# Optimization experiments

Hardware: AMD Instinct MI355X
Metric: run time of the kernel (lower is better)

Reference implementation:

```python
import jax, jax.numpy as jnp
import numpy as np

B, T, IN, H, OUT = 128, 1024, 17, 512, 17


def setup_inputs() -> dict:
    key = jax.random.key(0)
    ks = jax.random.split(key, 11)
    s_in = 1.0 / np.sqrt(H)
    return {
        "x": jax.random.normal(ks[0], (B, T, IN), dtype=jnp.float32),
        "wih0": jax.random.normal(ks[1], (4 * H, IN), dtype=jnp.float32) * s_in,
        "whh0": jax.random.normal(ks[2], (4 * H, H), dtype=jnp.float32) * s_in,
        "bih0": jax.random.normal(ks[3], (4 * H,), dtype=jnp.float32) * s_in,
        "bhh0": jax.random.normal(ks[4], (4 * H,), dtype=jnp.float32) * s_in,
        "wih1": jax.random.normal(ks[5], (4 * H, H), dtype=jnp.float32) * s_in,
        "whh1": jax.random.normal(ks[6], (4 * H, H), dtype=jnp.float32) * s_in,
        "bih1": jax.random.normal(ks[7], (4 * H,), dtype=jnp.float32) * s_in,
        "bhh1": jax.random.normal(ks[8], (4 * H,), dtype=jnp.float32) * s_in,
        "lin_w": jax.random.normal(ks[9], (OUT, H), dtype=jnp.float32) * s_in,
        "lin_b": jax.random.normal(ks[10], (OUT,), dtype=jnp.float32) * s_in,
    }


def _lstm_layer(x, wih, whh, bih, bhh):
    # x: [B, T, D]; gate order i, f, g, o (torch.nn.LSTMCell convention)
    b, _, _ = x.shape
    h = whh.shape[1]
    # Precompute input projection for all timesteps: [B, T, 4H]
    proj = jnp.einsum("btd,gd->btg", x, wih) + bih

    def step(carry, p_t):
        h_t, c_t = carry
        gates = p_t + h_t @ whh.T + bhh  # [B, 4H]
        i, f, g, o = jnp.split(gates, 4, axis=1)
        i = jax.nn.sigmoid(i)
        f = jax.nn.sigmoid(f)
        o = jax.nn.sigmoid(o)
        g = jnp.tanh(g)
        c_t = f * c_t + i * g
        h_t = o * jnp.tanh(c_t)
        return (h_t, c_t), h_t

    h0 = jnp.zeros((b, h), x.dtype)
    c0 = jnp.zeros((b, h), x.dtype)
    _, ys = jax.lax.scan(step, (h0, c0), jnp.swapaxes(proj, 0, 1))  # ys: [T, B, H]
    return jnp.swapaxes(ys, 0, 1)  # [B, T, H]


def reference(x, wih0, whh0, bih0, bhh0, wih1, whh1, bih1, bhh1, lin_w, lin_b):
    y = _lstm_layer(x, wih0, whh0, bih0, bhh0)
    y = _lstm_layer(y, wih1, whh1, bih1, bhh1)
    h_last = y[:, -1, :]  # [B, H]
    return h_last @ lin_w.T + lin_b  # [B, OUT]
```

## Files before the change

kernel.cpp:

```cpp
#include <hip/hip_runtime.h>
#include <cstddef>
#include <cstdint>

typedef unsigned long long ull;
typedef unsigned short u16;
typedef unsigned int u32;
typedef __attribute__((ext_vector_type(8))) short s8v;
typedef __attribute__((ext_vector_type(4))) float f4v;
typedef __attribute__((ext_vector_type(4))) u32 u32x4;

#define GROUPS 8
#define BG     16
#define JS     16
#define TPB    256
#define NT     1024
#define HDIM   512
#define INDIM  17
#define OUTDIM 17
#define BTOT   128

#define AT_LD(p)   __hip_atomic_load((p), __ATOMIC_RELAXED, __HIP_MEMORY_SCOPE_AGENT)
#define AT_ST(p,v) __hip_atomic_store((p), (v), __ATOMIC_RELAXED, __HIP_MEMORY_SCOPE_AGENT)

#define PLANE32 8192
#define WIDX(k, b) ((((k) >> 5) * 512) + ((((k) >> 3) & 3) * 128) + ((b) * 8) + ((k) & 7))

#define RA_OFF     ((size_t)0)
#define RING_BYTES ((size_t)4 * GROUPS * PLANE32 * 4)
#define RB_OFF     (RA_OFF + RING_BYTES)
#define FB32_OFF   (RB_OFF + RING_BYTES)
#define WS_NEEDED  (FB32_OFF + (size_t)BTOT * HDIM * 4)
#define RIX32(sl, gr) (((size_t)(sl) * GROUPS + (gr)) * PLANE32)

#define L_H0   0
#define L_H1   49152
#define L_CTL  65536
#define LDS_SZ 82944

__device__ __forceinline__ u16 f2bf(float f) {
  unsigned int u = __float_as_uint(f);
  u += 0x7FFFu + ((u >> 16) & 1u);
  return (u16)(u >> 16);
}
__device__ __forceinline__ float bf2f(u16 h) {
  return __uint_as_float(((unsigned int)h) << 16);
}
__device__ __forceinline__ float sigm(float x) { return 1.f / (1.f + __expf(-x)); }
__device__ __forceinline__ float tanh_f(float x) { return 2.f / (1.f + __expf(-2.f * x)) - 1.f; }

#define MFMA(a, b, c) __builtin_amdgcn_mfma_f32_16x16x32_bf16((a), (b), (c), 0, 0, 0)

__device__ __forceinline__ ull sc0_read8(const ull* p) {
  ull w;
  asm volatile("global_load_dwordx2 %0, %1, off sc0\n\ts_waitcnt vmcnt(0)"
               : "=&v"(w) : "v"(p) : "memory");
  return w;
}
__device__ __forceinline__ void sc0_read16(const char* base, u32x4 r[16]) {
  asm volatile(
      "global_load_dwordx4 %0, %16, off sc0\n\t"
      "global_load_dwordx4 %1, %16, off offset:1024 sc0\n\t"
      "global_load_dwordx4 %2, %16, off offset:2048 sc0\n\t"
      "global_load_dwordx4 %3, %16, off offset:3072 sc0\n\t"
      "global_load_dwordx4 %4, %17, off sc0\n\t"
      "global_load_dwordx4 %5, %17, off offset:1024 sc0\n\t"
      "global_load_dwordx4 %6, %17, off offset:2048 sc0\n\t"
      "global_load_dwordx4 %7, %17, off offset:3072 sc0\n\t"
      "global_load_dwordx4 %8, %18, off sc0\n\t"
      "global_load_dwordx4 %9, %18, off offset:1024 sc0\n\t"
      "global_load_dwordx4 %10, %18, off offset:2048 sc0\n\t"
      "global_load_dwordx4 %11, %18, off offset:3072 sc0\n\t"
      "global_load_dwordx4 %12, %19, off sc0\n\t"
      "global_load_dwordx4 %13, %19, off offset:1024 sc0\n\t"
      "global_load_dwordx4 %14, %19, off offset:2048 sc0\n\t"
      "global_load_dwordx4 %15, %19, off offset:3072 sc0\n\t"
      "s_waitcnt vmcnt(0)"
      : "=&v"(r[0]), "=&v"(r[1]), "=&v"(r[2]), "=&v"(r[3]),
        "=&v"(r[4]), "=&v"(r[5]), "=&v"(r[6]), "=&v"(r[7]),
        "=&v"(r[8]), "=&v"(r[9]), "=&v"(r[10]), "=&v"(r[11]),
        "=&v"(r[12]), "=&v"(r[13]), "=&v"(r[14]), "=&v"(r[15])
      : "v"(base), "v"(base + 4096), "v"(base + 8192), "v"(base + 12288)
      : "memory");
}

__device__ __forceinline__ void pbar(int* c, int& nbar, int lane) {
  ++nbar;
  if (lane == 0)
    (void)__hip_atomic_fetch_add(c, 1, __ATOMIC_RELEASE, __HIP_MEMORY_SCOPE_WORKGROUP);
  while (__hip_atomic_load(c, __ATOMIC_ACQUIRE, __HIP_MEMORY_SCOPE_WORKGROUP) < 2 * nbar) {}
}

__global__ __launch_bounds__(TPB, 1) void lstm_fused(
    const float* __restrict__ x,
    const float* __restrict__ wih0, const float* __restrict__ whh0,
    const float* __restrict__ bih0, const float* __restrict__ bhh0,
    const float* __restrict__ wih1, const float* __restrict__ whh1,
    const float* __restrict__ bih1, const float* __restrict__ bhh1,
    u32* __restrict__ ringA, u32* __restrict__ ringB,
    float* __restrict__ fb32)
{
  const int bid  = blockIdx.x;
  const int gr   = bid & 7;
  const int wg   = bid >> 3;
  const int j0   = wg * JS;
  const int tid  = threadIdx.x;
  const int wave = tid >> 6;
  const int lane = tid & 63;
  const int n    = lane & 15;
  const int q    = lane >> 4;
  const int k0   = q * 8;
  const int gidx = n & 3;
  const int jl   = n >> 2;

  __shared__ __align__(16) char smem[LDS_SZ];
  int* ctl = (int*)(smem + L_CTL);

  if (tid < 16) ctl[tid] = 0;

  {
    int b_l = tid >> 4, j_l = tid & 15, jgw = j0 + j_l;
    int wo = WIDX(jgw, b_l);
    AT_ST(&ringA[RIX32(0, gr) + wo], 0u);
    AT_ST(&ringB[RIX32(0, gr) + wo], 0u);
  }
  __syncthreads();

  const f4v z = {0.f, 0.f, 0.f, 0.f};
  const int half = wave & 1;
  const int sub = (lane >> 2) * 128 + (lane & 3) * 32;
  const ull TMASK = 0xFFFF0000FFFF0000ULL;

  if (wave < 2) {
    int jown[2];
    float bias[2][4];
    s8v wxh[2], wxl[2];
    s8v whh_[2][16], whl_[2][16];
#pragma unroll
    for (int i = 0; i < 2; ++i) {
      const int jc = wave * 2 + i;
      jown[i] = j0 + jc * 4 + q;
      const float* wr = wih0 + (size_t)(gidx * HDIM + j0 + jc * 4 + jl) * INDIM;
#pragma unroll
      for (int j = 0; j < 8; ++j) {
        int k = k0 + j;
        float v = (k < INDIM) ? wr[k] : 0.f;
        u16 hi = f2bf(v);
        wxh[i][j] = (short)hi;
        wxl[i][j] = (short)f2bf(v - bf2f(hi));
      }
      const float* hr = whh0 + (size_t)(gidx * HDIM + j0 + jc * 4 + jl) * HDIM;
#pragma unroll
      for (int kt = 0; kt < 16; ++kt)
#pragma unroll
        for (int j = 0; j < 8; ++j) {
          float v = hr[kt * 32 + k0 + j];
          u16 hi = f2bf(v);
          whh_[i][kt][j] = (short)hi;
          whl_[i][kt][j] = (short)f2bf(v - bf2f(hi));
        }
#pragma unroll
      for (int g = 0; g < 4; ++g)
        bias[i][g] = bih0[g * HDIM + jown[i]] + bhh0[g * HDIM + jown[i]];
    }
    float cc[2] = {0.f, 0.f};
    int nbar = 0, fast = 1, miss = 0;

    for (int s = 1; s <= NT + 1; ++s) {
      f4v xa[2] = {z, z};
      if (s <= NT) {
        const float* xr = x + ((size_t)(gr * BG + n) * NT + (s - 1)) * INDIM;
        s8v bxh, bxl;
#pragma unroll
        for (int j = 0; j < 8; ++j) {
          int k = k0 + j;
          float v = (k < INDIM) ? xr[k] : 0.f;
          u16 hi = f2bf(v);
          bxh[j] = (short)hi;
          bxl[j] = (short)f2bf(v - bf2f(hi));
        }
#pragma unroll
        for (int i = 0; i < 2; ++i) {
          xa[i] = MFMA(wxh[i], bxh, xa[i]);
          xa[i] = MFMA(wxh[i], bxl, xa[i]);
          xa[i] = MFMA(wxl[i], bxh, xa[i]);
        }
      }
      const int sl3 = (s - 1) % 3;
      {
        const ull* src = (const ull*)(ringA + RIX32((s - 1) & 3, gr)) + half * 2048;
        const ull tg = (ull)(u16)(s - 1);
        const ull pat = (tg << 16) | (tg << 48);
        int it = 0;
        for (;;) {
          ull w;
          if (fast && ((++it) & 7) != 0) w = sc0_read8(src + sub);
          else                           w = AT_LD(src + sub);
          int l1a = __hip_atomic_load(&ctl[7], __ATOMIC_ACQUIRE,
                                      __HIP_MEMORY_SCOPE_WORKGROUP);
          int l1b = __hip_atomic_load(&ctl[8], __ATOMIC_ACQUIRE,
                                      __HIP_MEMORY_SCOPE_WORKGROUP);
          int l1t = l1a < l1b ? l1a : l1b;
          if (__ballot((((w ^ pat) & TMASK) == 0) & (l1t >= s - 4)) == ~0ULL) break;
          if (!fast) __builtin_amdgcn_s_sleep(1);
        }
        u32x4 r[16];
        bool got = false;
        if (fast) {
#pragma unroll 1
          for (int att = 0; att < 2 && !got; ++att) {
            sc0_read16((const char*)src + lane * 16, r);
            ull acc = 0;
#pragma unroll
            for (int i = 0; i < 16; ++i) {
              ull a = ((ull)r[i][1] << 32) | r[i][0];
              ull b = ((ull)r[i][3] << 32) | r[i][2];
              acc |= (a ^ pat) & TMASK;
              acc |= (b ^ pat) & TMASK;
            }
            got = (__ballot(acc == 0) == ~0ULL);
          }
          miss = got ? 0 : miss + 1;
          if (miss >= 4) fast = 0;
        }
        if (!got) {
          for (;;) {
            ull acc = 0;
#pragma unroll
            for (int i = 0; i < 16; ++i) {
              ull a = AT_LD(src + (i * 64 + lane) * 2);
              ull b = AT_LD(src + (i * 64 + lane) * 2 + 1);
              r[i][0] = (u32)a; r[i][1] = (u32)(a >> 32);
              r[i][2] = (u32)b; r[i][3] = (u32)(b >> 32);
              acc |= (a ^ pat) & TMASK;
              acc |= (b ^ pat) & TMASK;
            }
            if (__ballot(acc == 0) == ~0ULL) break;
            __builtin_amdgcn_s_sleep(1);
          }
        }
        char* dst = smem + L_H0 + sl3 * 16384 + half * 8192;
#pragma unroll
        for (int i = 0; i < 16; ++i) {
          ull a = ((ull)r[i][1] << 32) | r[i][0];
          ull b = ((ull)r[i][3] << 32) | r[i][2];
          ull packed = (a & 0xFFFFULL) | ((a >> 16) & 0xFFFF0000ULL)
                     | ((b & 0xFFFFULL) << 32) | (((b >> 16) & 0xFFFF0000ULL) << 32);
          *(ull*)(dst + (i * 64 + lane) * 8) = packed;
        }
      }
      pbar(&ctl[0], nbar, lane);
      if (wave == 0 && lane == 0)
        __hip_atomic_store(&ctl[4 + sl3], s - 1, __ATOMIC_RELEASE,
                           __HIP_MEMORY_SCOPE_WORKGROUP);
      if (s == NT + 1) break;

      const char* sh = smem + L_H0 + sl3 * 16384;
      f4v cHH[2] = {z, z}, cHL[2] = {z, z};
#pragma unroll
      for (int kt = 0; kt < 16; ++kt) {
        s8v bh = *(const s8v*)(sh + kt * 1024 + q * 256 + n * 16);
#pragma unroll
        for (int i = 0; i < 2; ++i) {
          cHH[i] = MFMA(whh_[i][kt], bh, cHH[i]);
          cHL[i] = MFMA(whl_[i][kt], bh, cHL[i]);
        }
      }
      const u32 otag = ((u32)(u16)s) << 16;
      u32* d = ringA + RIX32(s & 3, gr);
#pragma unroll
      for (int ii = 1; ii >= 0; --ii) {
        f4v e = xa[ii] + cHH[ii] + cHL[ii];
        float pi = e[0] + bias[ii][0], pf = e[1] + bias[ii][1];
        float pg = e[2] + bias[ii][2], po = e[3] + bias[ii][3];
        float ig = sigm(pi), fg = sigm(pf), gv = tanh_f(pg), og = sigm(po);
        cc[ii] = fg * cc[ii] + ig * gv;
        AT_ST(d + WIDX(jown[ii], n), otag | (u32)f2bf(og * tanh_f(cc[ii])));
      }
    }
  } else {
    int jown[2];
    float bias[2][4];
    s8v w1x_[2][16], w1h_[2][16];
#pragma unroll
    for (int i = 0; i < 2; ++i) {
      const int jc = (wave - 2) * 2 + i;
      jown[i] = j0 + jc * 4 + q;
      const float* p1 = wih1 + (size_t)(gidx * HDIM + j0 + jc * 4 + jl) * HDIM;
      const float* p2 = whh1 + (size_t)(gidx * HDIM + j0 + jc * 4 + jl) * HDIM;
#pragma unroll
      for (int kt = 0; kt < 16; ++kt)
#pragma unroll
        for (int j = 0; j < 8; ++j) {
          w1x_[i][kt][j] = (short)f2bf(p1[kt * 32 + k0 + j]);
          w1h_[i][kt][j] = (short)f2bf(p2[kt * 32 + k0 + j]);
        }
#pragma unroll
      for (int g = 0; g < 4; ++g)
        bias[i][g] = bih1[g * HDIM + jown[i]] + bhh1[g * HDIM + jown[i]];
    }
    float c1[2] = {0.f, 0.f};
    int nbar = 0, fast = 1, miss = 0;

    for (int t = 1; t <= NT; ++t) {
      {
        const ull* src = (const ull*)(ringB + RIX32((t - 1) & 3, gr)) + half * 2048;
        const ull tg = (ull)(u16)(t - 1);
        const ull pat = (tg << 16) | (tg << 48);
        int it = 0;
        for (;;) {
          ull w;
          if (fast && ((++it) & 7) != 0) w = sc0_read8(src + sub);
          else                           w = AT_LD(src + sub);
          if (__ballot(((w ^ pat) & TMASK) == 0) == ~0ULL) break;
          if (!fast) __builtin_amdgcn_s_sleep(1);
        }
        u32x4 r[16];
        bool got = false;
        if (fast) {
#pragma unroll 1
          for (int att = 0; att < 2 && !got; ++att) {
            sc0_read16((const char*)src + lane * 16, r);
            ull acc = 0;
#pragma unroll
            for (int i = 0; i < 16; ++i) {
              ull a = ((ull)r[i][1] << 32) | r[i][0];
              ull b = ((ull)r[i][3] << 32) | r[i][2];
              acc |= (a ^ pat) & TMASK;
              acc |= (b ^ pat) & TMASK;
            }
            got = (__ballot(acc == 0) == ~0ULL);
          }
          miss = got ? 0 : miss + 1;
          if (miss >= 4) fast = 0;
        }
        if (!got) {
          for (;;) {
            ull acc = 0;
#pragma unroll
            for (int i = 0; i < 16; ++i) {
              ull a = AT_LD(src + (i * 64 + lane) * 2);
              ull b = AT_LD(src + (i * 64 + lane) * 2 + 1);
              r[i][0] = (u32)a; r[i][1] = (u32)(a >> 32);
              r[i][2] = (u32)b; r[i][3] = (u32)(b >> 32);
              acc |= (a ^ pat) & TMASK;
              acc |= (b ^ pat) & TMASK;
            }
            if (__ballot(acc == 0) == ~0ULL) break;
            __builtin_amdgcn_s_sleep(1);
          }
        }
        char* dst = smem + L_H1 + half * 8192;
#pragma unroll
        for (int i = 0; i < 16; ++i) {
          ull a = ((ull)r[i][1] << 32) | r[i][0];
          ull b = ((ull)r[i][3] << 32) | r[i][2];
          ull packed = (a & 0xFFFFULL) | ((a >> 16) & 0xFFFF0000ULL)
                     | ((b & 0xFFFFULL) << 32) | (((b >> 16) & 0xFFFF0000ULL) << 32);
          *(ull*)(dst + (i * 64 + lane) * 8) = packed;
        }
      }
      pbar(&ctl[1], nbar, lane);
      const char* th = smem + L_H1;
      f4v dHH[2] = {z, z};
#pragma unroll
      for (int kt = 0; kt < 16; ++kt) {
        s8v bh = *(const s8v*)(th + kt * 1024 + q * 256 + n * 16);
#pragma unroll
        for (int i = 0; i < 2; ++i) dHH[i] = MFMA(w1h_[i][kt], bh, dHH[i]);
      }
      const int sl3 = t % 3;
      while (__hip_atomic_load(&ctl[4 + sl3], __ATOMIC_ACQUIRE,
                               __HIP_MEMORY_SCOPE_WORKGROUP) < t) {}
      const char* sh = smem + L_H0 + sl3 * 16384;
      f4v eHH[2] = {z, z};
#pragma unroll
      for (int kt = 0; kt < 16; ++kt) {
        s8v bh = *(const s8v*)(sh + kt * 1024 + q * 256 + n * 16);
#pragma unroll
        for (int i = 0; i < 2; ++i) eHH[i] = MFMA(w1x_[i][kt], bh, eHH[i]);
      }
      if (lane == 0)
        __hip_atomic_store(&ctl[7 + (wave & 1)], t, __ATOMIC_RELEASE,
                           __HIP_MEMORY_SCOPE_WORKGROUP);
      const u32 otag = ((u32)(u16)t) << 16;
      u32* d = ringB + RIX32(t & 3, gr);
#pragma unroll
      for (int ii = 1; ii >= 0; --ii) {
        f4v e = dHH[ii] + eHH[ii];
        float pi = e[0] + bias[ii][0], pf = e[1] + bias[ii][1];
        float pg = e[2] + bias[ii][2], po = e[3] + bias[ii][3];
        float ig = sigm(pi), fg = sigm(pf), gv = tanh_f(pg), og = sigm(po);
        c1[ii] = fg * c1[ii] + ig * gv;
        float h = og * tanh_f(c1[ii]);
        AT_ST(d + WIDX(jown[ii], n), otag | (u32)f2bf(h));
        if (t == NT)
          AT_ST((u32*)&fb32[(size_t)(gr * BG + n) * HDIM + jown[ii]],
                __float_as_uint(h));
      }
    }
  }
}

__global__ void final_linear(const float* __restrict__ fb32,
                             const float* __restrict__ lin_w,
                             const float* __restrict__ lin_b,
                             float* __restrict__ out) {
  int b = blockIdx.x, o = threadIdx.x;
  if (o < OUTDIM) {
    float acc = lin_b[o];
    const u32* hr = (const u32*)(fb32 + (size_t)b * HDIM);
    for (int j = 0; j < HDIM; ++j) {
      float h = __uint_as_float(AT_LD(hr + j));
      acc += h * lin_w[(size_t)o * HDIM + j];
    }
    out[b * OUTDIM + o] = acc;
  }
}

__global__ void sentinel_kernel(float* __restrict__ out, int nv) {
  int i = blockIdx.x * TPB + threadIdx.x;
  if (i < nv) out[i] = 1e30f;
}

extern "C" void kernel_launch(void* const* d_in, const int* in_sizes, int n_in,
                              void* d_out, int out_size, void* d_ws, size_t ws_size,
                              hipStream_t stream) {
  (void)in_sizes; (void)n_in;
  const float* x     = (const float*)d_in[0];
  const float* wih0  = (const float*)d_in[1];
  const float* whh0  = (const float*)d_in[2];
  const float* bih0  = (const float*)d_in[3];
  const float* bhh0  = (const float*)d_in[4];
  const float* wih1  = (const float*)d_in[5];
  const float* whh1  = (const float*)d_in[6];
  const float* bih1  = (const float*)d_in[7];
  const float* bhh1  = (const float*)d_in[8];
  const float* lin_w = (const float*)d_in[9];
  const float* lin_b = (const float*)d_in[10];
  float* out = (float*)d_out;
  char* ws = (char*)d_ws;

  if (ws_size < WS_NEEDED) {
    sentinel_kernel<<<(out_size + TPB - 1) / TPB, TPB, 0, stream>>>(out, out_size);
    return;
  }

  u32* ringA  = (u32*)(ws + RA_OFF);
  u32* ringB  = (u32*)(ws + RB_OFF);
  float* fb32 = (float*)(ws + FB32_OFF);

  lstm_fused<<<256, TPB, 0, stream>>>(x, wih0, whh0, bih0, bhh0,
                                      wih1, whh1, bih1, bhh1,
                                      ringA, ringB, fb32);
  final_linear<<<BTOT, 64, 0, stream>>>(fb32, lin_w, lin_b, out);
}
```

Measured before the change: 5.696 ms.

## Stage hidden-state publishes through LDS and drop sc0 fast-path polling

Each wave now writes its gate outputs into a small per-wave LDS staging area and then publishes them to the global ring with one coalesced 64-bit atomic store per lane. Before, each lane issued scattered 32-bit atomic stores. The inline-asm sc0 read fast path and its miss-tracking fallback are removed, so polling always uses plain relaxed atomic loads with s_sleep backoff. This is meant to cut the count and scatter of cross-block global writes on the per-step critical path. The cost is an extra LDS round trip plus a waitcnt in every step, and possibly slower consumer polling without the sc0 loads.

```diff
diff --git a/kernel.cpp b/kernel.cpp
--- a/kernel.cpp
+++ b/kernel.cpp
@@ -7,7 +7,6 @@
 typedef unsigned int u32;
 typedef __attribute__((ext_vector_type(8))) short s8v;
 typedef __attribute__((ext_vector_type(4))) float f4v;
-typedef __attribute__((ext_vector_type(4))) u32 u32x4;
 
 #define GROUPS 8
 #define BG     16
@@ -34,7 +33,8 @@
 
 #define L_H0   0
 #define L_H1   49152
-#define L_CTL  65536
+#define L_STG  65536
+#define L_CTL  67584
 #define LDS_SZ 82944
 
 __device__ __forceinline__ u16 f2bf(float f) {
@@ -49,39 +49,6 @@
 __device__ __forceinline__ float tanh_f(float x) { return 2.f / (1.f + __expf(-2.f * x)) - 1.f; }
 
 #define MFMA(a, b, c) __builtin_amdgcn_mfma_f32_16x16x32_bf16((a), (b), (c), 0, 0, 0)
-
-__device__ __forceinline__ ull sc0_read8(const ull* p) {
-  ull w;
-  asm volatile("global_load_dwordx2 %0, %1, off sc0\n\ts_waitcnt vmcnt(0)"
-               : "=&v"(w) : "v"(p) : "memory");
-  return w;
-}
-__device__ __forceinline__ void sc0_read16(const char* base, u32x4 r[16]) {
-  asm volatile(
-      "global_load_dwordx4 %0, %16, off sc0\n\t"
-      "global_load_dwordx4 %1, %16, off offset:1024 sc0\n\t"
-      "global_load_dwordx4 %2, %16, off offset:2048 sc0\n\t"
-      "global_load_dwordx4 %3, %16, off offset:3072 sc0\n\t"
-      "global_load_dwordx4 %4, %17, off sc0\n\t"
-      "global_load_dwordx4 %5, %17, off offset:1024 sc0\n\t"
-      "global_load_dwordx4 %6, %17, off offset:2048 sc0\n\t"
-      "global_load_dwordx4 %7, %17, off offset:3072 sc0\n\t"
-      "global_load_dwordx4 %8, %18, off sc0\n\t"
-      "global_load_dwordx4 %9, %18, off offset:1024 sc0\n\t"
-      "global_load_dwordx4 %10, %18, off offset:2048 sc0\n\t"
-      "global_load_dwordx4 %11, %18, off offset:3072 sc0\n\t"
-      "global_load_dwordx4 %12, %19, off sc0\n\t"
-      "global_load_dwordx4 %13, %19, off offset:1024 sc0\n\t"
-      "global_load_dwordx4 %14, %19, off offset:2048 sc0\n\t"
-      "global_load_dwordx4 %15, %19, off offset:3072 sc0\n\t"
-      "s_waitcnt vmcnt(0)"
-      : "=&v"(r[0]), "=&v"(r[1]), "=&v"(r[2]), "=&v"(r[3]),
-        "=&v"(r[4]), "=&v"(r[5]), "=&v"(r[6]), "=&v"(r[7]),
-        "=&v"(r[8]), "=&v"(r[9]), "=&v"(r[10]), "=&v"(r[11]),
-        "=&v"(r[12]), "=&v"(r[13]), "=&v"(r[14]), "=&v"(r[15])
-      : "v"(base), "v"(base + 4096), "v"(base + 8192), "v"(base + 12288)
-      : "memory");
-}
 
 __device__ __forceinline__ void pbar(int* c, int& nbar, int lane) {
   ++nbar;
@@ -114,6 +81,7 @@
 
   __shared__ __align__(16) char smem[LDS_SZ];
   int* ctl = (int*)(smem + L_CTL);
+  u32* stg = (u32*)(smem + L_STG + (wave & 1) * 512 + (wave >> 1) * 1024);
 
   if (tid < 16) ctl[tid] = 0;
 
@@ -127,6 +95,7 @@
 
   const f4v z = {0.f, 0.f, 0.f, 0.f};
   const int half = wave & 1;
+  const int pub = (wg >> 1) * 256 + ((wg & 1) * 2 + (wave & 1)) * 64;
   const int sub = (lane >> 2) * 128 + (lane & 3) * 32;
   const ull TMASK = 0xFFFF0000FFFF0000ULL;
 
@@ -163,7 +132,7 @@
         bias[i][g] = bih0[g * HDIM + jown[i]] + bhh0[g * HDIM + jown[i]];
     }
     float cc[2] = {0.f, 0.f};
-    int nbar = 0, fast = 1, miss = 0;
+    int nbar = 0;
 
     for (int s = 1; s <= NT + 1; ++s) {
       f4v xa[2] = {z, z};
@@ -190,59 +159,33 @@
         const ull* src = (const ull*)(ringA + RIX32((s - 1) & 3, gr)) + half * 2048;
         const ull tg = (ull)(u16)(s - 1);
         const ull pat = (tg << 16) | (tg << 48);
-        int it = 0;
         for (;;) {
-          ull w;
-          if (fast && ((++it) & 7) != 0) w = sc0_read8(src + sub);
-          else                           w = AT_LD(src + sub);
+          ull w = AT_LD(src + sub);
           int l1a = __hip_atomic_load(&ctl[7], __ATOMIC_ACQUIRE,
                                       __HIP_MEMORY_SCOPE_WORKGROUP);
           int l1b = __hip_atomic_load(&ctl[8], __ATOMIC_ACQUIRE,
                                       __HIP_MEMORY_SCOPE_WORKGROUP);
           int l1t = l1a < l1b ? l1a : l1b;
           if (__ballot((((w ^ pat) & TMASK) == 0) & (l1t >= s - 4)) == ~0ULL) break;
-          if (!fast) __builtin_amdgcn_s_sleep(1);
-        }
-        u32x4 r[16];
-        bool got = false;
-        if (fast) {
-#pragma unroll 1
-          for (int att = 0; att < 2 && !got; ++att) {
-            sc0_read16((const char*)src + lane * 16, r);
-            ull acc = 0;
-#pragma unroll
-            for (int i = 0; i < 16; ++i) {
-              ull a = ((ull)r[i][1] << 32) | r[i][0];
-              ull b = ((ull)r[i][3] << 32) | r[i][2];
-              acc |= (a ^ pat) & TMASK;
-              acc |= (b ^ pat) & TMASK;
-            }
-            got = (__ballot(acc == 0) == ~0ULL);
+          __builtin_amdgcn_s_sleep(1);
+        }
+        ull v[32];
+        for (;;) {
+          ull acc = 0;
+#pragma unroll
+          for (int i = 0; i < 16; ++i) {
+            v[2 * i]     = AT_LD(src + (i * 64 + lane) * 2);
+            v[2 * i + 1] = AT_LD(src + (i * 64 + lane) * 2 + 1);
           }
-          miss = got ? 0 : miss + 1;
-          if (miss >= 4) fast = 0;
-        }
-        if (!got) {
-          for (;;) {
-            ull acc = 0;
-#pragma unroll
-            for (int i = 0; i < 16; ++i) {
-              ull a = AT_LD(src + (i * 64 + lane) * 2);
-              ull b = AT_LD(src + (i * 64 + lane) * 2 + 1);
-              r[i][0] = (u32)a; r[i][1] = (u32)(a >> 32);
-              r[i][2] = (u32)b; r[i][3] = (u32)(b >> 32);
-              acc |= (a ^ pat) & TMASK;
-              acc |= (b ^ pat) & TMASK;
-            }
-            if (__ballot(acc == 0) == ~0ULL) break;
-            __builtin_amdgcn_s_sleep(1);
-          }
+#pragma unroll
+          for (int i = 0; i < 32; ++i) acc |= (v[i] ^ pat) & TMASK;
+          if (__ballot(acc == 0) == ~0ULL) break;
+          __builtin_amdgcn_s_sleep(1);
         }
         char* dst = smem + L_H0 + sl3 * 16384 + half * 8192;
 #pragma unroll
         for (int i = 0; i < 16; ++i) {
-          ull a = ((ull)r[i][1] << 32) | r[i][0];
-          ull b = ((ull)r[i][3] << 32) | r[i][2];
+          ull a = v[2 * i], b = v[2 * i + 1];
           ull packed = (a & 0xFFFFULL) | ((a >> 16) & 0xFFFF0000ULL)
                      | ((b & 0xFFFFULL) << 32) | (((b >> 16) & 0xFFFF0000ULL) << 32);
           *(ull*)(dst + (i * 64 + lane) * 8) = packed;
@@ -266,15 +209,21 @@
         }
       }
       const u32 otag = ((u32)(u16)s) << 16;
-      u32* d = ringA + RIX32(s & 3, gr);
-#pragma unroll
-      for (int ii = 1; ii >= 0; --ii) {
+#pragma unroll
+      for (int ii = 0; ii < 2; ++ii) {
         f4v e = xa[ii] + cHH[ii] + cHL[ii];
         float pi = e[0] + bias[ii][0], pf = e[1] + bias[ii][1];
         float pg = e[2] + bias[ii][2], po = e[3] + bias[ii][3];
         float ig = sigm(pi), fg = sigm(pf), gv = tanh_f(pg), og = sigm(po);
         cc[ii] = fg * cc[ii] + ig * gv;
-        AT_ST(d + WIDX(jown[ii], n), otag | (u32)f2bf(og * tanh_f(cc[ii])));
+        stg[n * 8 + ii * 4 + q] = otag | (u32)f2bf(og * tanh_f(cc[ii]));
+      }
+      asm volatile("s_waitcnt lgkmcnt(0)" ::: "memory");
+      __builtin_amdgcn_sched_barrier(0);
+      {
+        ull v0 = *(const ull*)((const char*)stg + lane * 8);
+        ull* d = (ull*)(ringA + RIX32(s & 3, gr)) + pub;
+        AT_ST(d + lane, v0);
       }
     }
   } else {
@@ -299,61 +248,35 @@
         bias[i][g] = bih1[g * HDIM + jown[i]] + bhh1[g * HDIM + jown[i]];
     }
     float c1[2] = {0.f, 0.f};
-    int nbar = 0, fast = 1, miss = 0;
+    int nbar = 0;
 
     for (int t = 1; t <= NT; ++t) {
       {
         const ull* src = (const ull*)(ringB + RIX32((t - 1) & 3, gr)) + half * 2048;
         const ull tg = (ull)(u16)(t - 1);
         const ull pat = (tg << 16) | (tg << 48);
-        int it = 0;
         for (;;) {
-          ull w;
-          if (fast && ((++it) & 7) != 0) w = sc0_read8(src + sub);
-          else                           w = AT_LD(src + sub);
+          ull w = AT_LD(src + sub);
           if (__ballot(((w ^ pat) & TMASK) == 0) == ~0ULL) break;
-          if (!fast) __builtin_amdgcn_s_sleep(1);
-        }
-        u32x4 r[16];
-        bool got = false;
-        if (fast) {
-#pragma unroll 1
-          for (int att = 0; att < 2 && !got; ++att) {
-            sc0_read16((const char*)src + lane * 16, r);
-            ull acc = 0;
-#pragma unroll
-            for (int i = 0; i < 16; ++i) {
-              ull a = ((ull)r[i][1] << 32) | r[i][0];
-              ull b = ((ull)r[i][3] << 32) | r[i][2];
-              acc |= (a ^ pat) & TMASK;
-              acc |= (b ^ pat) & TMASK;
-            }
-            got = (__ballot(acc == 0) == ~0ULL);
+          __builtin_amdgcn_s_sleep(1);
+        }
+        ull v[32];
+        for (;;) {
+          ull acc = 0;
+#pragma unroll
+          for (int i = 0; i < 16; ++i) {
+            v[2 * i]     = AT_LD(src + (i * 64 + lane) * 2);
+            v[2 * i + 1] = AT_LD(src + (i * 64 + lane) * 2 + 1);
           }
-          miss = got ? 0 : miss + 1;
-          if (miss >= 4) fast = 0;
-        }
-        if (!got) {
-          for (;;) {
-            ull acc = 0;
-#pragma unroll
-            for (int i = 0; i < 16; ++i) {
-              ull a = AT_LD(src + (i * 64 + lane) * 2);
-              ull b = AT_LD(src + (i * 64 + lane) * 2 + 1);
-              r[i][0] = (u32)a; r[i][1] = (u32)(a >> 32);
-              r[i][2] = (u32)b; r[i][3] = (u32)(b >> 32);
-              acc |= (a ^ pat) & TMASK;
-              acc |= (b ^ pat) & TMASK;
-            }
-            if (__ballot(acc == 0) == ~0ULL) break;
-            __builtin_amdgcn_s_sleep(1);
-          }
+#pragma unroll
+          for (int i = 0; i < 32; ++i) acc |= (v[i] ^ pat) & TMASK;
+          if (__ballot(acc == 0) == ~0ULL) break;
+          __builtin_amdgcn_s_sleep(1);
         }
         char* dst = smem + L_H1 + half * 8192;
 #pragma unroll
         for (int i = 0; i < 16; ++i) {
-          ull a = ((ull)r[i][1] << 32) | r[i][0];
-          ull b = ((ull)r[i][3] << 32) | r[i][2];
+          ull a = v[2 * i], b = v[2 * i + 1];
           ull packed = (a & 0xFFFFULL) | ((a >> 16) & 0xFFFF0000ULL)
                      | ((b & 0xFFFFULL) << 32) | (((b >> 16) & 0xFFFF0000ULL) << 32);
           *(ull*)(dst + (i * 64 + lane) * 8) = packed;
@@ -383,19 +306,29 @@
         __hip_atomic_store(&ctl[7 + (wave & 1)], t, __ATOMIC_RELEASE,
                            __HIP_MEMORY_SCOPE_WORKGROUP);
       const u32 otag = ((u32)(u16)t) << 16;
-      u32* d = ringB + RIX32(t & 3, gr);
-#pragma unroll
-      for (int ii = 1; ii >= 0; --ii) {
+      float hout[2];
+#pragma unroll
+      for (int ii = 0; ii < 2; ++ii) {
         f4v e = dHH[ii] + eHH[ii];
         float pi = e[0] + bias[ii][0], pf = e[1] + bias[ii][1];
         float pg = e[2] + bias[ii][2], po = e[3] + bias[ii][3];
         float ig = sigm(pi), fg = sigm(pf), gv = tanh_f(pg), og = sigm(po);
         c1[ii] = fg * c1[ii] + ig * gv;
-        float h = og * tanh_f(c1[ii]);
-        AT_ST(d + WIDX(jown[ii], n), otag | (u32)f2bf(h));
-        if (t == NT)
+        hout[ii] = og * tanh_f(c1[ii]);
+        stg[n * 8 + ii * 4 + q] = otag | (u32)f2bf(hout[ii]);
+      }
+      asm volatile("s_waitcnt lgkmcnt(0)" ::: "memory");
+      __builtin_amdgcn_sched_barrier(0);
+      {
+        ull v0 = *(const ull*)((const char*)stg + lane * 8);
+        ull* d = (ull*)(ringB + RIX32(t & 3, gr)) + pub;
+        AT_ST(d + lane, v0);
+      }
+      if (t == NT) {
+#pragma unroll
+        for (int ii = 0; ii < 2; ++ii)
           AT_ST((u32*)&fb32[(size_t)(gr * BG + n) * HDIM + jown[ii]],
-                __float_as_uint(h));
+                __float_as_uint(hout[ii]));
       }
     }
   }
```

Measured after the change: 4.962 ms. 1.15x faster.
